# Optimization experiments

Measured on AMD Instinct MI355X. Metric: run time of the kernel, lower is better.

The kernel has to match this reference:

```python
import jax, jax.numpy as jnp
import numpy as np

INPUT_SHAPE = 640
NUM_CLASSES = 80
STRIDES = (8, 16, 32)
DIS = 2.5 * STRIDES[0]        # center-region half-size (pixels)
EPS = 1e-7
BIG = 1e5                      # penalty for non-(center&inbox) candidates
INF = 1e9                      # effectively excludes a pair from top-k / argmin
BS, MAX_GT, NGT_VALID = 32, 50, 20


def _bce(p, t):
    p = jnp.clip(p, EPS, 1.0 - EPS)
    return -t * jnp.log(p) - (1.0 - t) * jnp.log(1.0 - p)


def _decode(pred, stride):
    # pred [B, 5+nc, l, l] -> decoded [B, l*l, 5+nc] with boxes in pixels (cx,cy,w,h)
    B, C, l, _ = pred.shape
    p = jnp.transpose(pred, (0, 2, 3, 1))          # [B, l, l, C] (row=y, col=x)
    xy = jax.nn.sigmoid(p[..., :2])
    wh = p[..., 2:4]
    objcls = jax.nn.sigmoid(p[..., 4:])
    gx = jnp.arange(l, dtype=p.dtype)[None, :]      # ix varies along width
    gy = jnp.arange(l, dtype=p.dtype)[:, None]      # iy varies along height
    x = (gx + xy[..., 0]) * stride
    y = (gy + xy[..., 1]) * stride
    w = jnp.exp(wh[..., 0]) * stride
    h = jnp.exp(wh[..., 1]) * stride
    out = jnp.concatenate([jnp.stack([x, y, w, h], -1), objcls], -1)
    return out.reshape(B, l * l, C)


def _pairwise_iou(gt, pr):
    # gt [G,4], pr [A,4] in cxcywh -> [G,A]
    g_tl = gt[:, None, :2] - gt[:, None, 2:4] * 0.5
    g_br = gt[:, None, :2] + gt[:, None, 2:4] * 0.5
    p_tl = pr[None, :, :2] - pr[None, :, 2:4] * 0.5
    p_br = pr[None, :, :2] + pr[None, :, 2:4] * 0.5
    wh = jnp.maximum(jnp.minimum(g_br, p_br) - jnp.maximum(g_tl, p_tl), 0.0)
    inter = wh[..., 0] * wh[..., 1]
    union = gt[:, None, 2] * gt[:, None, 3] + pr[None, :, 2] * pr[None, :, 3] - inter
    return inter / jnp.clip(union, 1e-6)


def _region_mask(px, py, cx, cy, hw, hh):
    # anchor center inside (clipped) box around (cx,cy) with half-extents (hw,hh)
    left = jnp.maximum(cx - hw, 0.0)[:, None]
    right = jnp.minimum(cx + hw, float(INPUT_SHAPE))[:, None]
    top = jnp.maximum(cy - hh, 0.0)[:, None]
    bot = jnp.minimum(cy + hh, float(INPUT_SHAPE))[:, None]
    return (px[None] >= left) & (px[None] <= right) & (py[None] >= top) & (py[None] <= bot)


def _per_image(pred, tgt):
    # pred [A, 5+nc] decoded, tgt [G, 5+nc]
    G, A = tgt.shape[0], pred.shape[0]
    valid = tgt[:, 4] == 1.0
    px, py = pred[:, 0], pred[:, 1]
    cx, cy, gw, gh = tgt[:, 0], tgt[:, 1], tgt[:, 2], tgt[:, 3]

    center_m = _region_mask(px, py, cx, cy, DIS, DIS)
    inbox_m = _region_mask(px, py, cx, cy, gw * 0.5, gh * 0.5)
    or_m = (center_m | inbox_m) & valid[:, None]     # candidate anchors
    and_m = center_m & inbox_m & valid[:, None]      # preferred anchors

    iou = _pairwise_iou(tgt[:, :4], pred[:, :4])     # [G, A]
    iou_cost = -jnp.log(iou + 1e-8)

    # pairwise class BCE cost summed over classes, via matmul (one-hot targets)
    pcls = jnp.clip(pred[:, 5:], EPS, 1.0 - EPS)     # [A, nc]
    logp = jnp.log(pcls)
    log1mp = jnp.log(1.0 - pcls)
    tcls = tgt[:, 5:]                                 # [G, nc]
    cls_cost = tcls @ (log1mp - logp).T - log1mp.sum(-1)[None, :]  # [G, A]

    cost = cls_cost + 3.0 * iou_cost + BIG * (~and_m)
    cost_full = jnp.where(valid[:, None], cost, INF)
    cost_sel = jnp.where(or_m, cost, INF)

    # dynamic-k: sum of top-10 candidate IoUs, floored at 1, capped by #and-candidates
    k10 = jax.lax.top_k(iou * or_m.astype(iou.dtype), 10)[0].sum(-1)
    and_cnt = and_m.sum(-1)
    dk = jnp.minimum(jnp.maximum(k10.astype(jnp.int32), 1), jnp.maximum(and_cnt, 1))

    # take 10 lowest-cost anchors per GT, keep the first dk of them
    _, topi = jax.lax.top_k(-cost_sel, 10)            # [G, 10]
    keep = (jnp.arange(10)[None, :] < dk[:, None]) & valid[:, None]
    keep = keep & jnp.take_along_axis(or_m, topi, axis=1)
    assign = jnp.zeros((G, A), jnp.int32).at[jnp.arange(G)[:, None], topi].max(
        keep.astype(jnp.int32)) > 0                    # [G, A] bool

    overlap = assign.sum(0) > 1
    best = jnp.argmin(cost_full, axis=0)              # [A]
    onehot = jnp.arange(G)[:, None] == best[None, :]
    assign = jnp.where(overlap[None, :], onehot, assign)

    fg = assign.any(0)
    l_conf = _bce(pred[:, 4], fg.astype(pred.dtype)).sum()
    l_cls = jnp.sum(jnp.where(assign, cls_cost, 0.0))
    l_reg = jnp.sum(jnp.where(assign, 1.0 - iou ** 2, 0.0))
    return l_reg, l_conf, l_cls, valid.sum()


def setup_inputs() -> dict:
    key = jax.random.key(0)
    k1, k2, k3, k4, k5, k6, k7 = jax.random.split(key, 7)
    p8 = 0.5 * jax.random.normal(k1, (BS, 5 + NUM_CLASSES, 80, 80), jnp.float32)
    p16 = 0.5 * jax.random.normal(k2, (BS, 5 + NUM_CLASSES, 40, 40), jnp.float32)
    p32 = 0.5 * jax.random.normal(k3, (BS, 5 + NUM_CLASSES, 20, 20), jnp.float32)
    # targets: (cx, cy, w, h, valid_flag, one_hot_class)
    cxy = jax.random.uniform(k4, (BS, NGT_VALID, 2), jnp.float32, 32.0, INPUT_SHAPE - 32.0)
    wh = jax.random.uniform(k5, (BS, NGT_VALID, 2), jnp.float32, 16.0, 128.0)
    cls_idx = jax.random.randint(k6, (BS, NGT_VALID), 0, NUM_CLASSES)
    onehot = jax.nn.one_hot(cls_idx, NUM_CLASSES, dtype=jnp.float32)
    flag = jnp.ones((BS, NGT_VALID, 1), jnp.float32)
    valid_rows = jnp.concatenate([cxy, wh, flag, onehot], -1)   # [BS, 20, 85]
    pad = jnp.zeros((BS, MAX_GT - NGT_VALID, 5 + NUM_CLASSES), jnp.float32)
    targets = jnp.concatenate([valid_rows, pad], axis=1)        # [BS, 50, 85]
    return {"p8": p8, "p16": p16, "p32": p32, "targets": targets}


def reference(p8, p16, p32, targets):
    preds = jnp.concatenate(
        [_decode(p8, STRIDES[0]), _decode(p16, STRIDES[1]), _decode(p32, STRIDES[2])],
        axis=1)                                                  # [BS, 8400, 85]
    l_reg, l_conf, l_cls, ng = jax.vmap(_per_image)(preds, targets)
    num_gts = jnp.maximum(ng.sum(), 1).astype(preds.dtype)
    reg_weight = 5.0
    return (reg_weight * l_reg.sum() + l_cls.sum() + l_conf.sum()) / num_gts
```

## Files before the change

### kernel.cpp

```cpp
#include <hip/hip_runtime.h>
#include <math.h>

#define BSZ  32
#define GSZ  50
#define ATOT 8400
#define NCLS 80
#define CDIM 85
#define TPB  256
#define TPA  512
#define GRIDX ((ATOT + TPB - 1) / TPB)
#define NPART (GRIDX * BSZ)
#define MAXC 512

#define EPSF 1e-7f
#define BIGF 100000.0f
#define INFF 1000000000.0f
#define IMGF 640.0f
#define DISF 20.0f
#define LOGEPS_HI -15.942385f
#define LN2F 0.69314718056f

__device__ __forceinline__ float fexp(float x){ return __expf(x); }
__device__ __forceinline__ float flog(float x){ return __logf(x); }

__device__ __forceinline__ float sigm(float z){ return 1.0f/(1.0f+fexp(-z)); }
__device__ __forceinline__ float clampp(float s){ return fminf(fmaxf(s, EPSF), 1.f-EPSF); }

__device__ __forceinline__ float l1ms2(float z){
  return fmaxf(-__log2f(1.f + fexp(z)), -23.0f);
}
__device__ __forceinline__ void acc2(float4& A, float4 w){
  A.x += l1ms2(w.x); A.y += l1ms2(w.y);
  A.z += l1ms2(w.z); A.w += l1ms2(w.w);
}

__device__ __forceinline__ const float* chan_ptr(const float* __restrict__ p8,
                                                 const float* __restrict__ p16,
                                                 const float* __restrict__ p32,
                                                 int b, int a, int ch){
  if (a < 6400) return p8  + ((size_t)(b*CDIM + ch))*6400 + a;
  if (a < 8000) return p16 + ((size_t)(b*CDIM + ch))*1600 + (a-6400);
  return p32 + ((size_t)(b*CDIM + ch))*400 + (a-8000);
}

__device__ __forceinline__ void compute_pair(
  float cx, float cy, float gw, float gh,
  float px, float py, float pw, float ph,
  float z, float slog,
  float& cost, float& iou, bool& orm, bool& andm, float& clsc)
{
  float hw = gw*0.5f, hh = gh*0.5f;
  bool cm = (px >= fmaxf(cx-DISF,0.f)) && (px <= fminf(cx+DISF,IMGF)) &&
            (py >= fmaxf(cy-DISF,0.f)) && (py <= fminf(cy+DISF,IMGF));
  bool im = (px >= fmaxf(cx-hw,0.f)) && (px <= fminf(cx+hw,IMGF)) &&
            (py >= fmaxf(cy-hh,0.f)) && (py <= fminf(cy+hh,IMGF));
  orm = cm || im;  andm = cm && im;
  float phw = pw*0.5f, phh = ph*0.5f;
  float wx = fmaxf(fminf(cx+hw, px+phw) - fmaxf(cx-hw, px-phw), 0.f);
  float wy = fmaxf(fminf(cy+hh, py+phh) - fmaxf(cy-hh, py-phh), 0.f);
  float inter = wx*wy;
  float uni   = gw*gh + pw*ph - inter;
  iou = inter / fmaxf(uni, 1e-6f);
  clsc = -z - slog;
  cost = clsc + 3.f*(-flog(iou + 1e-8f)) + (andm ? 0.f : BIGF);
}

__global__ __launch_bounds__(TPB, 4)
void k_decode(const float* __restrict__ p8, const float* __restrict__ p16,
              const float* __restrict__ p32, const float* __restrict__ tgt,
              float* __restrict__ bx, float* __restrict__ by,
              float* __restrict__ bw, float* __restrict__ bh,
              float* __restrict__ obj, float* __restrict__ slog,
              unsigned long long* __restrict__ bits, int* __restrict__ cidx,
              int* __restrict__ vflag){
  int t = blockIdx.x*blockDim.x + threadIdx.x;
  int sub = t & 3;
  int g   = t >> 2;
  int b = g / (ATOT/4);
  int q = g % (ATOT/4);
  int a0 = q*4;
  const float* base; int l; float fs; int aL; int ii, jj;
  if (a0 < 6400){ base = p8;  l = 80; fs = 8.f;  aL = a0;      ii = aL/80; jj = aL - ii*80; }
  else if (a0 < 8000){ base = p16; l = 40; fs = 16.f; aL = a0-6400; ii = aL/40; jj = aL - ii*40; }
  else { base = p32; l = 20; fs = 32.f; aL = a0-8000; ii = aL/20; jj = aL - ii*20; }
  int l2 = l*l;
  int cs = l2 >> 2;
  const float4* p4 = (const float4*)(base + (size_t)b*CDIM*l2) + (aL >> 2);

  float4 vA = p4[(size_t)sub*cs];
  float4 vB = p4[(size_t)4*cs];

  const float4* cp = p4 + (size_t)(5+sub)*cs;
  const size_t st4 = (size_t)4*cs;
  float4 A0 = make_float4(0.f,0.f,0.f,0.f);
  float4 A1 = A0, A2 = A0, A3 = A0;
  float4 w0 = cp[0], w1 = cp[st4], w2 = cp[2*st4], w3 = cp[3*st4];
  #pragma unroll
  for (int k = 0; k < 20; k += 4){
    float4 n0, n1, n2, n3;
    if (k + 4 < 20){
      n0 = cp[(size_t)(k+4)*st4];
      n1 = cp[(size_t)(k+5)*st4];
      n2 = cp[(size_t)(k+6)*st4];
      n3 = cp[(size_t)(k+7)*st4];
    }
    acc2(A0, w0); acc2(A1, w1); acc2(A2, w2); acc2(A3, w3);
    if (k + 4 < 20){ w0 = n0; w1 = n1; w2 = n2; w3 = n3; }
  }
  float4 S = make_float4(A0.x+A1.x+A2.x+A3.x, A0.y+A1.y+A2.y+A3.y,
                         A0.z+A1.z+A2.z+A3.z, A0.w+A1.w+A2.w+A3.w);
  #pragma unroll
  for (int m = 1; m <= 2; m <<= 1){
    S.x += __shfl_xor(S.x, m, 64);
    S.y += __shfl_xor(S.y, m, 64);
    S.z += __shfl_xor(S.z, m, 64);
    S.w += __shfl_xor(S.w, m, 64);
  }

  float fi = (float)ii;
  uint4 z4 = make_uint4(0u,0u,0u,0u);
  if (sub == 0){
    ((float4*)bx)[g]  = make_float4(((float)(jj  )+sigm(vA.x))*fs, ((float)(jj+1)+sigm(vA.y))*fs,
                                    ((float)(jj+2)+sigm(vA.z))*fs, ((float)(jj+3)+sigm(vA.w))*fs);
    ((float4*)obj)[g] = make_float4(sigm(vB.x), sigm(vB.y), sigm(vB.z), sigm(vB.w));
    ((uint4*)bits)[2*g] = z4;
  } else if (sub == 1){
    ((float4*)by)[g]   = make_float4((fi+sigm(vA.x))*fs, (fi+sigm(vA.y))*fs,
                                     (fi+sigm(vA.z))*fs, (fi+sigm(vA.w))*fs);
    ((float4*)slog)[g] = make_float4(S.x*LN2F, S.y*LN2F, S.z*LN2F, S.w*LN2F);
  } else if (sub == 2){
    ((float4*)bw)[g] = make_float4(fexp(vA.x)*fs, fexp(vA.y)*fs, fexp(vA.z)*fs, fexp(vA.w)*fs);
    ((uint4*)bits)[2*g+1] = z4;
  } else {
    ((float4*)bh)[g] = make_float4(fexp(vA.x)*fs, fexp(vA.y)*fs, fexp(vA.z)*fs, fexp(vA.w)*fs);
  }

  if (t < BSZ*GSZ){
    const float* Tq = tgt + (size_t)t*CDIM;
    int best = 0; float bv = Tq[5];
    for (int c = 1; c < NCLS; c++){
      float vv = Tq[5+c];
      if (vv > bv){ bv = vv; best = c; }
    }
    cidx[t] = best;
    vflag[t] = (Tq[4] == 1.0f) ? 1 : 0;
  }
}

__device__ __forceinline__ unsigned f2u(float f){
  unsigned u = __float_as_uint(f);
  return (u & 0x80000000u) ? ~u : (u | 0x80000000u);
}

__global__ __launch_bounds__(TPA)
void k_assign(const float* __restrict__ p8, const float* __restrict__ p16,
              const float* __restrict__ p32, const float* __restrict__ tgt,
              const int* __restrict__ cidx,
              const float* __restrict__ bx, const float* __restrict__ by,
              const float* __restrict__ bw, const float* __restrict__ bh,
              const float* __restrict__ slog,
              unsigned long long* __restrict__ bits){
  int g = blockIdx.x, b = blockIdx.y;
  const float* T = tgt + ((size_t)b*GSZ + g)*CDIM;
  if (T[4] != 1.0f) return;
  float cx = T[0], cy = T[1], gw = T[2], gh = T[3];
  float hw = gw*0.5f, hh = gh*0.5f;
  float cL = fmaxf(cx-DISF,0.f), cR = fminf(cx+DISF,IMGF);
  float cT = fmaxf(cy-DISF,0.f), cB = fminf(cy+DISF,IMGF);
  float iL = fmaxf(cx-hw,0.f),  iR = fminf(cx+hw,IMGF);
  float iT = fmaxf(cy-hh,0.f),  iB = fminf(cy+hh,IMGF);
  float gArea = gw*gh;
  int ch = 5 + cidx[b*GSZ + g];
  int t = threadIdx.x;
  int lane = t & 63, wave = t >> 6;

  const float* BX = bx + (size_t)b*ATOT;
  const float* BY = by + (size_t)b*ATOT;
  const float* BW = bw + (size_t)b*ATOT;
  const float* BH = bh + (size_t)b*ATOT;
  const float* SL = slog + (size_t)b*ATOT;

  float ux = fmaxf(DISF, hw), uy = fmaxf(DISF, hh);
  float RL = fmaxf(cx-ux, 0.f), RR = fminf(cx+ux, IMGF);
  float RT = fmaxf(cy-uy, 0.f), RB = fminf(cy+uy, IMGF);

  auto rect = [&](float inv, int l, int& j0r, int& i0r, int& wr, int& hr){
    int a_ = (int)floorf(RL*inv) - 1; if (a_ < 0) a_ = 0;
    int b_ = (int)floorf(RR*inv) + 1; if (b_ > l-1) b_ = l-1;
    int c_ = (int)floorf(RT*inv) - 1; if (c_ < 0) c_ = 0;
    int d_ = (int)floorf(RB*inv) + 1; if (d_ > l-1) d_ = l-1;
    j0r = a_; i0r = c_; wr = b_-a_+1; hr = d_-c_+1;
  };
  int j0_0,i0_0,w_0,h_0, j0_1,i0_1,w_1,h_1, j0_2,i0_2,w_2,h_2;
  rect(0.125f,   80, j0_0,i0_0,w_0,h_0);
  rect(0.0625f,  40, j0_1,i0_1,w_1,h_1);
  rect(0.03125f, 20, j0_2,i0_2,w_2,h_2);
  int o1 = w_0*h_0, o2 = o1 + w_1*h_1, ntot = o2 + w_2*h_2;

  __shared__ int cand[MAXC];
  __shared__ int ncand_sh;
  __shared__ int wand[TPA/64];
  if (t == 0) ncand_sh = 0;
  __syncthreads();

  int myand = 0;
  for (int cell = t; cell < ntot; cell += TPA){
    int v = (cell >= o1) + (cell >= o2);
    int loc, jj0, ii0, ww, ll, ab;
    if (v == 0){ loc = cell;    jj0=j0_0; ii0=i0_0; ww=w_0; ll=80; ab=0;    }
    else if (v == 1){ loc = cell-o1; jj0=j0_1; ii0=i0_1; ww=w_1; ll=40; ab=6400; }
    else { loc = cell-o2; jj0=j0_2; ii0=i0_2; ww=w_2; ll=20; ab=8000; }
    int ii = ii0 + loc / ww;
    int jj = jj0 + loc % ww;
    int a  = ab + ii*ll + jj;
    float px = BX[a], py = BY[a];
    bool cm = (px >= cL) && (px <= cR) && (py >= cT) && (py <= cB);
    bool im = (px >= iL) && (px <= iR) && (py >= iT) && (py <= iB);
    bool orm = cm || im, andm = cm && im;
    unsigned long long mo = __ballot(orm);
    myand += __popcll(__ballot(andm));
    if (orm){
      int leader = __ffsll((long long)mo) - 1;
      int base = 0;
      if (lane == leader) base = atomicAdd(&ncand_sh, __popcll(mo));
      base = __shfl(base, leader, 64);
      int pos = base + __popcll(mo & ((1ull << lane) - 1ull));
      if (pos < MAXC) cand[pos] = a | (andm ? 0x10000 : 0);
    }
  }
  if (lane == 0) wand[wave] = myand;
  __syncthreads();
  int nc = ncand_sh < MAXC ? ncand_sh : MAXC;

  unsigned long long ck; float io;
  if (t < nc){
    int packed = cand[t];
    int a = packed & 0xFFFF;
    bool andm = (packed & 0x10000) != 0;
    float px = BX[a], py = BY[a];
    float pw = BW[a], ph = BH[a];
    float phw = pw*0.5f, phh = ph*0.5f;
    float wx = fmaxf(fminf(cx+hw, px+phw) - fmaxf(cx-hw, px-phw), 0.f);
    float wy = fmaxf(fminf(cy+hh, py+phh) - fmaxf(cy-hh, py-phh), 0.f);
    float inter = wx*wy;
    io = inter / fmaxf(gArea + pw*ph - inter, 1e-6f);
    float z = *chan_ptr(p8, p16, p32, b, a, ch);
    float cost = (-z - SL[a]) + 3.f*(-flog(io + 1e-8f)) + (andm ? 0.f : BIGF);
    ck = ((unsigned long long)f2u(cost) << 32) | (unsigned)a;
  } else {
    ck = ~0ull; io = -1.f;
  }

  __shared__ unsigned long long skey[(TPA/64)*10];
  __shared__ float siou[(TPA/64)*10];
  bool wactive = (wave << 6) < nc;
  if (wactive){
    #pragma unroll
    for (int k = 2; k <= 64; k <<= 1){
      #pragma unroll
      for (int j = k >> 1; j > 0; j >>= 1){
        unsigned long long ok = __shfl_xor(ck, j, 64);
        float oi = __shfl_xor(io, j, 64);
        bool tmin = (((lane & k) == 0) == ((lane & j) == 0));
        ck = tmin ? (ck < ok ? ck : ok) : (ck > ok ? ck : ok);
        io = tmin ? fmaxf(io, oi) : fminf(io, oi);
      }
    }
  }
  if (lane < 10){
    skey[wave*10 + lane] = wactive ? ck : ~0ull;
    siou[wave*10 + lane] = wactive ? io : -1.f;
  }
  __syncthreads();

  if (t == 0){
    int and_cnt = 0;
    #pragma unroll
    for (int q = 0; q < TPA/64; q++) and_cnt += wand[q];
    float k10 = 0.f;
    {
      int h[TPA/64] = {0,0,0,0,0,0,0,0};
      for (int r = 0; r < 10; r++){
        float v = -2.f; int w = -1;
        #pragma unroll
        for (int q = 0; q < TPA/64; q++){
          if (h[q] < 10){
            float vq = siou[q*10 + h[q]];
            if (vq > v){ v = vq; w = q; }
          }
        }
        if (w >= 0) h[w]++;
        k10 += fmaxf(v, 0.f);
      }
    }
    int dk = (int)k10;
    if (dk < 1) dk = 1;
    int ub = and_cnt > 1 ? and_cnt : 1;
    if (dk > ub) dk = ub;
    int h[TPA/64] = {0,0,0,0,0,0,0,0};
    for (int r = 0; r < dk && r < 10; r++){
      unsigned long long bestk = ~0ull; int w = -1;
      #pragma unroll
      for (int q = 0; q < TPA/64; q++){
        if (h[q] < 10){
          unsigned long long kq = skey[q*10 + h[q]];
          if (kq < bestk){ bestk = kq; w = q; }
        }
      }
      if (bestk == ~0ull) break;
      h[w]++;
      int idx = (int)(bestk & 0xFFFFFFFFull);
      atomicOr(&bits[(size_t)b*ATOT + idx], 1ull << g);
    }
  }
}

__global__ void k_loss(const float* __restrict__ p8, const float* __restrict__ p16,
                       const float* __restrict__ p32, const float* __restrict__ tgt,
                       const int* __restrict__ cidx,
                       const float* __restrict__ bx, const float* __restrict__ by,
                       const float* __restrict__ bw, const float* __restrict__ bh,
                       const float* __restrict__ obj, const float* __restrict__ slog,
                       const unsigned long long* __restrict__ bits,
                       float* __restrict__ partials){
  int b = blockIdx.y;
  int a = blockIdx.x*TPB + threadIdx.x;
  __shared__ float gcx[GSZ], gcy[GSZ], ggw[GSZ], ggh[GSZ], gval[GSZ];
  __shared__ int gci[GSZ];
  for (int k = threadIdx.x; k < GSZ; k += TPB){
    const float* T = tgt + ((size_t)b*GSZ + k)*CDIM;
    gcx[k] = T[0]; gcy[k] = T[1]; ggw[k] = T[2]; ggh[k] = T[3]; gval[k] = T[4];
    gci[k] = cidx[b*GSZ + k];
  }
  __syncthreads();

  float contrib = 0.f;
  if (a < ATOT){
    size_t t = (size_t)b*ATOT + a;
    unsigned long long m = bits[t];
    float o = clampp(obj[t]);
    if (m == 0ull){
      contrib = -flog(1.f - o);
    } else {
      float px = bx[t], py = by[t], pw = bw[t], ph = bh[t], sl = slog[t];
      if (__builtin_popcountll(m) > 1){
        float bestc = INFF; int bestg = 0;
        for (int g = 0; g < GSZ; g++){
          float c = INFF;
          if (gval[g] == 1.0f){
            float z = *chan_ptr(p8, p16, p32, b, a, 5+gci[g]);
            float iou, clsc; bool orm, andm;
            compute_pair(gcx[g], gcy[g], ggw[g], ggh[g], px, py, pw, ph, z, sl,
                         c, iou, orm, andm, clsc);
          }
          if (c < bestc){ bestc = c; bestg = g; }
        }
        m = 1ull << bestg;
      }
      contrib = -flog(o);
      while (m){
        int g = __builtin_ctzll(m);
        m &= m - 1;
        float z = *chan_ptr(p8, p16, p32, b, a, 5+gci[g]);
        float c, iou, clsc; bool orm, andm;
        compute_pair(gcx[g], gcy[g], ggw[g], ggh[g], px, py, pw, ph, z, sl,
                     c, iou, orm, andm, clsc);
        contrib += clsc + 5.f*(1.f - iou*iou);
      }
    }
  }

  #pragma unroll
  for (int s2 = 32; s2 > 0; s2 >>= 1) contrib += __shfl_xor(contrib, s2, 64);
  __shared__ float wsum[4];
  if ((threadIdx.x & 63) == 0) wsum[threadIdx.x >> 6] = contrib;
  __syncthreads();
  if (threadIdx.x == 0)
    partials[blockIdx.y*GRIDX + blockIdx.x] = wsum[0]+wsum[1]+wsum[2]+wsum[3];
}

__global__ void k_final(const float* __restrict__ partials,
                        const int* __restrict__ vflag, float* __restrict__ out){
  int t = threadIdx.x;
  float s = 0.f;
  for (int i = t; i < NPART; i += TPB) s += partials[i];
  int n = 0;
  for (int i = t; i < BSZ*GSZ; i += TPB) n += vflag[i];
  #pragma unroll
  for (int s2 = 32; s2 > 0; s2 >>= 1){
    s += __shfl_xor(s, s2, 64);
    n += __shfl_xor(n, s2, 64);
  }
  __shared__ float sh[4]; __shared__ int shn[4];
  if ((t & 63) == 0){ sh[t >> 6] = s; shn[t >> 6] = n; }
  __syncthreads();
  if (t == 0){
    float tot = sh[0]+sh[1]+sh[2]+sh[3];
    int nn = shn[0]+shn[1]+shn[2]+shn[3];
    if (nn < 1) nn = 1;
    out[0] = tot / (float)nn;
  }
}

extern "C" void kernel_launch(void* const* d_in, const int* in_sizes, int n_in,
                              void* d_out, int out_size, void* d_ws, size_t ws_size,
                              hipStream_t stream) {
  const float* p8  = (const float*)d_in[0];
  const float* p16 = (const float*)d_in[1];
  const float* p32 = (const float*)d_in[2];
  const float* tgt = (const float*)d_in[3];
  float* out = (float*)d_out;

  const size_t BA = (size_t)BSZ*ATOT;
  float* bx   = (float*)d_ws;
  float* by   = bx + BA;
  float* bw   = by + BA;
  float* bh   = bw + BA;
  float* obj  = bh + BA;
  float* slog = obj + BA;
  unsigned long long* bits = (unsigned long long*)(slog + BA);
  int* cidx = (int*)(bits + BA);
  float* partials = (float*)(cidx + BSZ*GSZ);
  int* vflag = (int*)(partials + NPART);

  dim3 blk(TPB);
  k_decode<<<dim3((unsigned)(BA/TPB)), blk, 0, stream>>>(p8, p16, p32, tgt,
                                                   bx, by, bw, bh, obj, slog, bits,
                                                   cidx, vflag);
  k_assign<<<dim3(GSZ, BSZ), dim3(TPA), 0, stream>>>(p8, p16, p32, tgt, cidx,
                                               bx, by, bw, bh, slog, bits);
  k_loss  <<<dim3(GRIDX, BSZ), blk, 0, stream>>>(p8, p16, p32, tgt, cidx,
                                               bx, by, bw, bh, obj, slog, bits, partials);
  k_final <<<1, blk, 0, stream>>>(partials, vflag, out);
}
```

Baseline: 152.2 us.

## Process all channels per thread in decode kernel, dropping channel-split shuffles

```diff
diff --git a/kernel.cpp b/kernel.cpp
--- a/kernel.cpp
+++ b/kernel.cpp
@@ -11,6 +11,7 @@
 #define GRIDX ((ATOT + TPB - 1) / TPB)
 #define NPART (GRIDX * BSZ)
 #define MAXC 512
+#define NG   (BSZ*(ATOT/4))
 
 #define EPSF 1e-7f
 #define BIGF 100000.0f
@@ -65,7 +66,7 @@
   cost = clsc + 3.f*(-flog(iou + 1e-8f)) + (andm ? 0.f : BIGF);
 }
 
-__global__ __launch_bounds__(TPB, 4)
+__global__ __launch_bounds__(TPB, 2)
 void k_decode(const float* __restrict__ p8, const float* __restrict__ p16,
               const float* __restrict__ p32, const float* __restrict__ tgt,
               float* __restrict__ bx, float* __restrict__ by,
@@ -74,65 +75,50 @@
               unsigned long long* __restrict__ bits, int* __restrict__ cidx,
               int* __restrict__ vflag){
   int t = blockIdx.x*blockDim.x + threadIdx.x;
-  int sub = t & 3;
-  int g   = t >> 2;
-  int b = g / (ATOT/4);
-  int q = g % (ATOT/4);
-  int a0 = q*4;
-  const float* base; int l; float fs; int aL; int ii, jj;
-  if (a0 < 6400){ base = p8;  l = 80; fs = 8.f;  aL = a0;      ii = aL/80; jj = aL - ii*80; }
-  else if (a0 < 8000){ base = p16; l = 40; fs = 16.f; aL = a0-6400; ii = aL/40; jj = aL - ii*40; }
-  else { base = p32; l = 20; fs = 32.f; aL = a0-8000; ii = aL/20; jj = aL - ii*20; }
-  int l2 = l*l;
-  int cs = l2 >> 2;
-  const float4* p4 = (const float4*)(base + (size_t)b*CDIM*l2) + (aL >> 2);
-
-  float4 vA = p4[(size_t)sub*cs];
-  float4 vB = p4[(size_t)4*cs];
-
-  const float4* cp = p4 + (size_t)(5+sub)*cs;
-  const size_t st4 = (size_t)4*cs;
-  float4 A0 = make_float4(0.f,0.f,0.f,0.f);
-  float4 A1 = A0, A2 = A0, A3 = A0;
-  float4 w0 = cp[0], w1 = cp[st4], w2 = cp[2*st4], w3 = cp[3*st4];
-  #pragma unroll
-  for (int k = 0; k < 20; k += 4){
-    float4 n0, n1, n2, n3;
-    if (k + 4 < 20){
-      n0 = cp[(size_t)(k+4)*st4];
-      n1 = cp[(size_t)(k+5)*st4];
-      n2 = cp[(size_t)(k+6)*st4];
-      n3 = cp[(size_t)(k+7)*st4];
-    }
-    acc2(A0, w0); acc2(A1, w1); acc2(A2, w2); acc2(A3, w3);
-    if (k + 4 < 20){ w0 = n0; w1 = n1; w2 = n2; w3 = n3; }
-  }
-  float4 S = make_float4(A0.x+A1.x+A2.x+A3.x, A0.y+A1.y+A2.y+A3.y,
-                         A0.z+A1.z+A2.z+A3.z, A0.w+A1.w+A2.w+A3.w);
-  #pragma unroll
-  for (int m = 1; m <= 2; m <<= 1){
-    S.x += __shfl_xor(S.x, m, 64);
-    S.y += __shfl_xor(S.y, m, 64);
-    S.z += __shfl_xor(S.z, m, 64);
-    S.w += __shfl_xor(S.w, m, 64);
-  }
-
-  float fi = (float)ii;
-  uint4 z4 = make_uint4(0u,0u,0u,0u);
-  if (sub == 0){
-    ((float4*)bx)[g]  = make_float4(((float)(jj  )+sigm(vA.x))*fs, ((float)(jj+1)+sigm(vA.y))*fs,
-                                    ((float)(jj+2)+sigm(vA.z))*fs, ((float)(jj+3)+sigm(vA.w))*fs);
-    ((float4*)obj)[g] = make_float4(sigm(vB.x), sigm(vB.y), sigm(vB.z), sigm(vB.w));
-    ((uint4*)bits)[2*g] = z4;
-  } else if (sub == 1){
-    ((float4*)by)[g]   = make_float4((fi+sigm(vA.x))*fs, (fi+sigm(vA.y))*fs,
-                                     (fi+sigm(vA.z))*fs, (fi+sigm(vA.w))*fs);
-    ((float4*)slog)[g] = make_float4(S.x*LN2F, S.y*LN2F, S.z*LN2F, S.w*LN2F);
-  } else if (sub == 2){
-    ((float4*)bw)[g] = make_float4(fexp(vA.x)*fs, fexp(vA.y)*fs, fexp(vA.z)*fs, fexp(vA.w)*fs);
-    ((uint4*)bits)[2*g+1] = z4;
-  } else {
-    ((float4*)bh)[g] = make_float4(fexp(vA.x)*fs, fexp(vA.y)*fs, fexp(vA.z)*fs, fexp(vA.w)*fs);
+  if (t < NG){
+    int b = t / (ATOT/4);
+    int q = t % (ATOT/4);
+    int a0 = q*4;
+    const float* base; int l; float fs; int aL; int ii, jj;
+    if (a0 < 6400){ base = p8;  l = 80; fs = 8.f;  aL = a0;      ii = aL/80; jj = aL - ii*80; }
+    else if (a0 < 8000){ base = p16; l = 40; fs = 16.f; aL = a0-6400; ii = aL/40; jj = aL - ii*40; }
+    else { base = p32; l = 20; fs = 32.f; aL = a0-8000; ii = aL/20; jj = aL - ii*20; }
+    int l2 = l*l;
+    int cs = l2 >> 2;
+    const float4* p4 = (const float4*)(base + (size_t)b*CDIM*l2) + (aL >> 2);
+
+    float4 v0 = p4[0];
+    float4 v1 = p4[(size_t)cs];
+    float4 v2 = p4[(size_t)2*cs];
+    float4 v3 = p4[(size_t)3*cs];
+    float4 v4 = p4[(size_t)4*cs];
+
+    const float4* cp = p4 + (size_t)5*cs;
+    float4 A0 = make_float4(0.f,0.f,0.f,0.f);
+    float4 A1 = A0, A2 = A0, A3 = A0;
+    #pragma unroll
+    for (int c = 0; c < 80; c += 4){
+      float4 w0 = cp[(size_t)(c+0)*cs];
+      float4 w1 = cp[(size_t)(c+1)*cs];
+      float4 w2 = cp[(size_t)(c+2)*cs];
+      float4 w3 = cp[(size_t)(c+3)*cs];
+      acc2(A0, w0); acc2(A1, w1); acc2(A2, w2); acc2(A3, w3);
+    }
+    float4 S = make_float4(A0.x+A1.x+A2.x+A3.x, A0.y+A1.y+A2.y+A3.y,
+                           A0.z+A1.z+A2.z+A3.z, A0.w+A1.w+A2.w+A3.w);
+
+    float fj = (float)jj, fi = (float)ii;
+    ((float4*)bx)[t]   = make_float4((fj    +sigm(v0.x))*fs, (fj+1.f+sigm(v0.y))*fs,
+                                     (fj+2.f+sigm(v0.z))*fs, (fj+3.f+sigm(v0.w))*fs);
+    ((float4*)by)[t]   = make_float4((fi+sigm(v1.x))*fs, (fi+sigm(v1.y))*fs,
+                                     (fi+sigm(v1.z))*fs, (fi+sigm(v1.w))*fs);
+    ((float4*)bw)[t]   = make_float4(fexp(v2.x)*fs, fexp(v2.y)*fs, fexp(v2.z)*fs, fexp(v2.w)*fs);
+    ((float4*)bh)[t]   = make_float4(fexp(v3.x)*fs, fexp(v3.y)*fs, fexp(v3.z)*fs, fexp(v3.w)*fs);
+    ((float4*)obj)[t]  = make_float4(sigm(v4.x), sigm(v4.y), sigm(v4.z), sigm(v4.w));
+    ((float4*)slog)[t] = make_float4(S.x*LN2F, S.y*LN2F, S.z*LN2F, S.w*LN2F);
+    uint4 z4 = make_uint4(0u,0u,0u,0u);
+    ((uint4*)bits)[2*t]   = z4;
+    ((uint4*)bits)[2*t+1] = z4;
   }
 
   if (t < BSZ*GSZ){
@@ -424,7 +410,7 @@
   int* vflag = (int*)(partials + NPART);
 
   dim3 blk(TPB);
-  k_decode<<<dim3((unsigned)(BA/TPB)), blk, 0, stream>>>(p8, p16, p32, tgt,
+  k_decode<<<dim3((NG + TPB - 1)/TPB), blk, 0, stream>>>(p8, p16, p32, tgt,
                                                    bx, by, bw, bh, obj, slog, bits,
                                                    cidx, vflag);
   k_assign<<<dim3(GSZ, BSZ), dim3(TPA), 0, stream>>>(p8, p16, p32, tgt, cidx,
```

Result: slower. 160.6 us (+5.5%).
